# Kernel tuning notes

Hardware: AMD Instinct MI355X
Metric: run time of the kernel (lower is better)

Reference implementation:

```python
import jax, jax.numpy as jnp
import numpy as np

MSG_DIM = 100
REG_WEIGHT = 1.0
N_NODES = 100000
N_EDGES = 1000000
D_FEAT = 6
HIDDEN = 300
OUT_DIM = 2


def setup_inputs() -> dict:
    key = jax.random.key(0)
    ks = jax.random.split(key, 10)
    def glorot(k, shape):
        fan_in = shape[0]
        return jax.random.normal(k, shape, dtype=jnp.float32) / jnp.sqrt(jnp.float32(fan_in))
    return {
        "x": jax.random.normal(ks[0], (N_NODES, D_FEAT), dtype=jnp.float32),
        "edge_index": jax.random.randint(ks[1], (2, N_EDGES), 0, N_NODES, dtype=jnp.int64)
            if jax.config.jax_enable_x64 else jax.random.randint(ks[1], (2, N_EDGES), 0, N_NODES, dtype=jnp.int32),
        "y": jax.random.normal(ks[2], (N_NODES, OUT_DIM), dtype=jnp.float32),
        "target": jax.random.normal(ks[3], (N_NODES, OUT_DIM), dtype=jnp.float32),
        "W1": glorot(ks[4], (2 * D_FEAT, HIDDEN)),
        "b1": jnp.zeros((HIDDEN,), dtype=jnp.float32),
        "W2": glorot(ks[5], (HIDDEN, HIDDEN)),
        "b2": jnp.zeros((HIDDEN,), dtype=jnp.float32),
        "W3": glorot(ks[6], (HIDDEN, 2 * MSG_DIM)),
        "b3": jnp.zeros((2 * MSG_DIM,), dtype=jnp.float32),
    }


def reference(x, edge_index, y, target, W1, b1, W2, b2, W3, b3):
    # MAE term: sum |y - target| / n_nodes
    base_loss = jnp.sum(jnp.abs(y - target)) / y.shape[0]
    # Gather sender/receiver node features per edge and concat -> [E, 2*d_feat]
    e = jnp.concatenate([x[edge_index[0]], x[edge_index[1]]], axis=1)
    # edge_model MLP: 2*d_feat -> 300 -> 300 -> 2*msg_dim
    h = jax.nn.relu(e @ W1 + b1)
    h = jax.nn.relu(h @ W2 + b2)
    messages = h @ W3 + b3  # [E, 2*msg_dim]
    mu = messages[:, :MSG_DIM]
    logvar = messages[:, MSG_DIM:]
    kl_reg = jnp.sum(0.5 * (mu * mu + jnp.exp(logvar) - logvar - 1.0)) / messages.shape[0]
    return base_loss + REG_WEIGHT * kl_reg
```

## Files before the change

kernel.cpp:

```cpp
#include <hip/hip_runtime.h>

#define N_NODES 100000
#define N_EDGES 1000000
#define D_FEAT  6
#define HIDDEN  300
#define HID_P   320
#define MSG     100
#define OUTC    200
#define OUTC_P  208
#define MT      64
#define NT_H    (HID_P/16)
#define NT_M    (OUTC_P/16)
#define KS_H    (HID_P/32)

typedef __bf16 bf16_t;
typedef __bf16 bf16x8 __attribute__((ext_vector_type(8)));
typedef float  floatx4 __attribute__((ext_vector_type(4)));

#define H_STRIDE  328
#define A1_STRIDE 40

#define PREP_BLOCKS 700
#define LOSS_BLOCKS 200
__global__ void prep_kernel(const float* __restrict__ W1, const float* __restrict__ W2,
                            const float* __restrict__ W3, bf16_t* __restrict__ W1P,
                            bf16_t* __restrict__ W2P, bf16_t* __restrict__ W3P,
                            const float* __restrict__ y, const float* __restrict__ t,
                            float* __restrict__ out) {
    if (blockIdx.x >= PREP_BLOCKS) {
        float s = 0.f;
        for (int i = (blockIdx.x - PREP_BLOCKS) * blockDim.x + threadIdx.x;
             i < N_NODES * 2; i += LOSS_BLOCKS * blockDim.x)
            s += fabsf(y[i] - t[i]);
        #pragma unroll
        for (int off = 32; off; off >>= 1) s += __shfl_down(s, off);
        __shared__ float red[4];
        if ((threadIdx.x & 63) == 0) red[threadIdx.x >> 6] = s;
        __syncthreads();
        if (threadIdx.x == 0)
            atomicAdd(out, (red[0] + red[1] + red[2] + red[3]) * (1.0f / N_NODES));
        return;
    }
    const int n1 = NT_H * 512;
    const int n2 = NT_H * KS_H * 512;
    const int n3 = NT_M * KS_H * 512;
    const int total = n1 + n2 + n3;
    for (int id = blockIdx.x * blockDim.x + threadIdx.x; id < total;
         id += PREP_BLOCKS * blockDim.x) {
        if (id < n1) {
            int nt = id >> 9, rem = id & 511, lane = rem >> 3, j = rem & 7;
            int n = nt * 16 + (lane & 15), k = (lane >> 4) * 8 + j;
            float v = (n < HIDDEN && k < 2 * D_FEAT) ? W1[k * HIDDEN + n] : 0.f;
            W1P[id] = (bf16_t)v;
        } else if (id < n1 + n2) {
            int r = id - n1;
            int chunk = r >> 9, rem = r & 511, lane = rem >> 3, j = rem & 7;
            int ks = chunk % KS_H, nt = chunk / KS_H;
            int n = nt * 16 + (lane & 15), k = ks * 32 + (lane >> 4) * 8 + j;
            float v = (n < HIDDEN && k < HIDDEN) ? W2[k * HIDDEN + n] : 0.f;
            W2P[r] = (bf16_t)v;
        } else {
            int r = id - n1 - n2;
            int chunk = r >> 9, rem = r & 511, lane = rem >> 3, j = rem & 7;
            int ks = chunk % KS_H, nt = chunk / KS_H;
            int n = nt * 16 + (lane & 15), k = ks * 32 + (lane >> 4) * 8 + j;
            float v = (n < OUTC && k < HIDDEN) ? W3[k * OUTC + n] : 0.f;
            W3P[r] = (bf16_t)v;
        }
    }
}

__global__ __launch_bounds__(512, 6) void mlp_kernel(
    const float* __restrict__ x, const int* __restrict__ ei,
    const bf16_t* __restrict__ W1P, const bf16_t* __restrict__ W2P,
    const bf16_t* __restrict__ W3P,
    const float* __restrict__ b1, const float* __restrict__ b2,
    const float* __restrict__ b3, float* __restrict__ out) {
    __shared__ __align__(16) bf16_t A1[MT * A1_STRIDE];
    __shared__ __align__(16) bf16_t H[MT * H_STRIDE];
    __shared__ float red[8];

    const int tid  = threadIdx.x;
    const int wave = tid >> 6, lane = tid & 63;
    const int quad = lane >> 4, l16 = lane & 15;
    const int wn = wave;
    const int cnt_h = (wn < 4) ? 3 : 2;
    const int cnt_m = (wn >= 3) ? 2 : 1;
    const long e0 = (long)blockIdx.x * MT;

    {
        uint* a32 = (uint*)A1;
        for (int i = tid; i < MT * A1_STRIDE / 2; i += 512) a32[i] = 0u;
    }
    __syncthreads();
    if (tid < 2 * MT) {
        int m = tid >> 1, side = tid & 1;
        int node = ei[(long)side * N_EDGES + e0 + m];
        const float* xr = x + (long)node * D_FEAT;
        bf16_t* dst = A1 + m * A1_STRIDE + side * D_FEAT;
        #pragma unroll
        for (int j = 0; j < D_FEAT; j++) dst[j] = (bf16_t)xr[j];
    }
    __syncthreads();

    floatx4 acc1[3][4];
    {
        bf16x8 a[4];
        #pragma unroll
        for (int mi = 0; mi < 4; mi++)
            a[mi] = *(const bf16x8*)&A1[(mi * 16 + l16) * A1_STRIDE + quad * 8];
        #pragma unroll
        for (int t = 0; t < 3; t++) {
            if (t < cnt_h) {
                int ntg = wn + 8 * t;
                bf16x8 b = *(const bf16x8*)&W1P[(ntg * 64 + lane) * 8];
                #pragma unroll
                for (int mi = 0; mi < 4; mi++) {
                    floatx4 z = {0.f, 0.f, 0.f, 0.f};
                    acc1[t][mi] = __builtin_amdgcn_mfma_f32_16x16x32_bf16(a[mi], b, z, 0, 0, 0);
                }
            }
        }
    }
    #pragma unroll
    for (int t = 0; t < 3; t++) {
        if (t < cnt_h) {
            int n = (wn + 8 * t) * 16 + l16;
            float bias = (n < HIDDEN) ? b1[n] : 0.f;
            #pragma unroll
            for (int mi = 0; mi < 4; mi++) {
                int mbase = mi * 16 + quad * 4;
                #pragma unroll
                for (int r = 0; r < 4; r++) {
                    float v = fmaxf(acc1[t][mi][r] + bias, 0.f);
                    H[(mbase + r) * H_STRIDE + n] = (bf16_t)v;
                }
            }
        }
    }
    __syncthreads();

    floatx4 acc2[3][4];
    #pragma unroll
    for (int t = 0; t < 3; t++)
        #pragma unroll
        for (int mi = 0; mi < 4; mi++) acc2[t][mi] = (floatx4){0.f, 0.f, 0.f, 0.f};
    #pragma unroll 2
    for (int ks = 0; ks < KS_H; ks++) {
        bf16x8 a[4];
        #pragma unroll
        for (int mi = 0; mi < 4; mi++)
            a[mi] = *(const bf16x8*)&H[(mi * 16 + l16) * H_STRIDE + ks * 32 + quad * 8];
        #pragma unroll
        for (int t = 0; t < 3; t++) {
            if (t < cnt_h) {
                int ntg = wn + 8 * t;
                bf16x8 b = *(const bf16x8*)&W2P[((ntg * KS_H + ks) * 64 + lane) * 8];
                #pragma unroll
                for (int mi = 0; mi < 4; mi++)
                    acc2[t][mi] = __builtin_amdgcn_mfma_f32_16x16x32_bf16(a[mi], b, acc2[t][mi], 0, 0, 0);
            }
        }
    }
    __syncthreads();
    #pragma unroll
    for (int t = 0; t < 3; t++) {
        if (t < cnt_h) {
            int n = (wn + 8 * t) * 16 + l16;
            float bias = (n < HIDDEN) ? b2[n] : 0.f;
            #pragma unroll
            for (int mi = 0; mi < 4; mi++) {
                int mbase = mi * 16 + quad * 4;
                #pragma unroll
                for (int r = 0; r < 4; r++) {
                    float v = fmaxf(acc2[t][mi][r] + bias, 0.f);
                    H[(mbase + r) * H_STRIDE + n] = (bf16_t)v;
                }
            }
        }
    }
    __syncthreads();

    floatx4 acc3[2][4];
    #pragma unroll
    for (int t = 0; t < 2; t++)
        #pragma unroll
        for (int mi = 0; mi < 4; mi++) acc3[t][mi] = (floatx4){0.f, 0.f, 0.f, 0.f};
    #pragma unroll 2
    for (int ks = 0; ks < KS_H; ks++) {
        bf16x8 a[4];
        #pragma unroll
        for (int mi = 0; mi < 4; mi++)
            a[mi] = *(const bf16x8*)&H[(mi * 16 + l16) * H_STRIDE + ks * 32 + quad * 8];
        #pragma unroll
        for (int t = 0; t < 2; t++) {
            if (t < cnt_m) {
                int ntg = wn + 5 * t;
                bf16x8 b = *(const bf16x8*)&W3P[((ntg * KS_H + ks) * 64 + lane) * 8];
                #pragma unroll
                for (int mi = 0; mi < 4; mi++)
                    acc3[t][mi] = __builtin_amdgcn_mfma_f32_16x16x32_bf16(a[mi], b, acc3[t][mi], 0, 0, 0);
            }
        }
    }
    float s = 0.f;
    #pragma unroll
    for (int t = 0; t < 2; t++) {
        if (t < cnt_m) {
            int n = (wn + 5 * t) * 16 + l16;
            if (n < OUTC) {
                float bias = b3[n];
                #pragma unroll
                for (int mi = 0; mi < 4; mi++)
                    #pragma unroll
                    for (int r = 0; r < 4; r++) {
                        float v = acc3[t][mi][r] + bias;
                        if (n < MSG) s += 0.5f * v * v;
                        else         s += 0.5f * (__expf(v) - v - 1.f);
                    }
            }
        }
    }
    #pragma unroll
    for (int off = 32; off; off >>= 1) s += __shfl_down(s, off);
    if (lane == 0) red[wave] = s;
    __syncthreads();
    if (tid == 0) {
        float t2 = 0.f;
        #pragma unroll
        for (int w = 0; w < 8; w++) t2 += red[w];
        atomicAdd(out, t2 * (1.0f / N_EDGES));
    }
}

extern "C" void kernel_launch(void* const* d_in, const int* in_sizes, int n_in,
                              void* d_out, int out_size, void* d_ws, size_t ws_size,
                              hipStream_t stream) {
    const float* x      = (const float*)d_in[0];
    const int*   ei     = (const int*)d_in[1];
    const float* y      = (const float*)d_in[2];
    const float* target = (const float*)d_in[3];
    const float* W1     = (const float*)d_in[4];
    const float* b1     = (const float*)d_in[5];
    const float* W2     = (const float*)d_in[6];
    const float* b2     = (const float*)d_in[7];
    const float* W3     = (const float*)d_in[8];
    const float* b3     = (const float*)d_in[9];
    float* out = (float*)d_out;

    bf16_t* W1P = (bf16_t*)d_ws;
    bf16_t* W2P = W1P + NT_H * 512;
    bf16_t* W3P = W2P + NT_H * KS_H * 512;

    hipMemsetAsync(d_out, 0, sizeof(float), stream);
    prep_kernel<<<PREP_BLOCKS + LOSS_BLOCKS, 256, 0, stream>>>(
        W1, W2, W3, W1P, W2P, W3P, y, target, out);
    mlp_kernel<<<N_EDGES / MT, 512, 0, stream>>>(x, ei, W1P, W2P, W3P, b1, b2, b3, out);
}
```

Before: 490.4 us.

## Store activations in MFMA fragment layout and swap operands to pack-store outputs

Swaps the MFMA operands so weights act as A and activations as B, making each lane hold four consecutive hidden columns. That allows bias to be read as a float4 and the ReLU outputs to be written to shared memory as packed bf16x4 stores. Activations are kept in a pre-swizzled fragment layout, so every layer reads one contiguous 16-byte chunk per lane instead of using padded-row strides. The goal is fewer shared-memory store instructions and fewer bank conflicts in the epilogues. The price is more complex index math, and the A1 zero-fill now covers only 2048 elements, which happens to match the new buffer size.

```diff
diff --git a/kernel.cpp b/kernel.cpp
--- a/kernel.cpp
+++ b/kernel.cpp
@@ -15,10 +15,8 @@
 
 typedef __bf16 bf16_t;
 typedef __bf16 bf16x8 __attribute__((ext_vector_type(8)));
+typedef __bf16 bf16x4 __attribute__((ext_vector_type(4)));
 typedef float  floatx4 __attribute__((ext_vector_type(4)));
-
-#define H_STRIDE  328
-#define A1_STRIDE 40
 
 #define PREP_BLOCKS 700
 #define LOSS_BLOCKS 200
@@ -76,48 +74,47 @@
     const bf16_t* __restrict__ W3P,
     const float* __restrict__ b1, const float* __restrict__ b2,
     const float* __restrict__ b3, float* __restrict__ out) {
-    __shared__ __align__(16) bf16_t A1[MT * A1_STRIDE];
-    __shared__ __align__(16) bf16_t H[MT * H_STRIDE];
+    __shared__ __align__(16) bf16_t A1f[4 * 64 * 8];
+    __shared__ __align__(16) bf16_t Hf[4 * KS_H * 64 * 8];
     __shared__ float red[8];
 
     const int tid  = threadIdx.x;
-    const int wave = tid >> 6, lane = tid & 63;
-    const int quad = lane >> 4, l16 = lane & 15;
-    const int wn = wave;
-    const int cnt_h = (wn < 4) ? 3 : 2;
-    const int cnt_m = (wn >= 3) ? 2 : 1;
+    const int w    = tid >> 6, lane = tid & 63;
+    const int q    = lane >> 4, l16 = lane & 15;
+    const int cnt_h = (w < 4) ? 3 : 2;
+    const int cnt_m = (w >= 3) ? 2 : 1;
     const long e0 = (long)blockIdx.x * MT;
 
-    {
-        uint* a32 = (uint*)A1;
-        for (int i = tid; i < MT * A1_STRIDE / 2; i += 512) a32[i] = 0u;
-    }
+    *(ulong*)&A1f[tid * 4] = 0ul;
     __syncthreads();
     if (tid < 2 * MT) {
         int m = tid >> 1, side = tid & 1;
         int node = ei[(long)side * N_EDGES + e0 + m];
         const float* xr = x + (long)node * D_FEAT;
-        bf16_t* dst = A1 + m * A1_STRIDE + side * D_FEAT;
-        #pragma unroll
-        for (int j = 0; j < D_FEAT; j++) dst[j] = (bf16_t)xr[j];
+        int et = m >> 4, ml = m & 15;
+        #pragma unroll
+        for (int c = 0; c < D_FEAT; c++) {
+            int k = side * D_FEAT + c;
+            int lp = ml + 16 * (k >> 3);
+            A1f[(et * 64 + lp) * 8 + (k & 7)] = (bf16_t)xr[c];
+        }
     }
     __syncthreads();
 
     floatx4 acc1[3][4];
     {
-        bf16x8 a[4];
-        #pragma unroll
-        for (int mi = 0; mi < 4; mi++)
-            a[mi] = *(const bf16x8*)&A1[(mi * 16 + l16) * A1_STRIDE + quad * 8];
+        bf16x8 hb[4];
+        #pragma unroll
+        for (int e = 0; e < 4; e++)
+            hb[e] = *(const bf16x8*)&A1f[(e * 64 + lane) * 8];
         #pragma unroll
         for (int t = 0; t < 3; t++) {
             if (t < cnt_h) {
-                int ntg = wn + 8 * t;
-                bf16x8 b = *(const bf16x8*)&W1P[(ntg * 64 + lane) * 8];
-                #pragma unroll
-                for (int mi = 0; mi < 4; mi++) {
+                bf16x8 wf = *(const bf16x8*)&W1P[((w + 8 * t) * 64 + lane) * 8];
+                #pragma unroll
+                for (int e = 0; e < 4; e++) {
                     floatx4 z = {0.f, 0.f, 0.f, 0.f};
-                    acc1[t][mi] = __builtin_amdgcn_mfma_f32_16x16x32_bf16(a[mi], b, z, 0, 0, 0);
+                    acc1[t][e] = __builtin_amdgcn_mfma_f32_16x16x32_bf16(wf, hb[e], z, 0, 0, 0);
                 }
             }
         }
@@ -125,16 +122,17 @@
     #pragma unroll
     for (int t = 0; t < 3; t++) {
         if (t < cnt_h) {
-            int n = (wn + 8 * t) * 16 + l16;
-            float bias = (n < HIDDEN) ? b1[n] : 0.f;
+            int n0 = (w + 8 * t) * 16 + 4 * q;
+            floatx4 bv = (n0 < HIDDEN) ? *(const floatx4*)&b1[n0]
+                                       : (floatx4){0.f, 0.f, 0.f, 0.f};
+            int ks = n0 >> 5, lp = l16 + 16 * ((n0 >> 3) & 3), j0 = n0 & 7;
             #pragma unroll
-            for (int mi = 0; mi < 4; mi++) {
-                int mbase = mi * 16 + quad * 4;
-                #pragma unroll
-                for (int r = 0; r < 4; r++) {
-                    float v = fmaxf(acc1[t][mi][r] + bias, 0.f);
-                    H[(mbase + r) * H_STRIDE + n] = (bf16_t)v;
-                }
+            for (int e = 0; e < 4; e++) {
+                bf16x4 pk;
+                #pragma unroll
+                for (int r = 0; r < 4; r++)
+                    pk[r] = (bf16_t)fmaxf(acc1[t][e][r] + bv[r], 0.f);
+                *(bf16x4*)&Hf[((e * KS_H + ks) * 64 + lp) * 8 + j0] = pk;
             }
         }
     }
@@ -144,21 +142,20 @@
     #pragma unroll
     for (int t = 0; t < 3; t++)
         #pragma unroll
-        for (int mi = 0; mi < 4; mi++) acc2[t][mi] = (floatx4){0.f, 0.f, 0.f, 0.f};
+        for (int e = 0; e < 4; e++) acc2[t][e] = (floatx4){0.f, 0.f, 0.f, 0.f};
     #pragma unroll 2
     for (int ks = 0; ks < KS_H; ks++) {
-        bf16x8 a[4];
-        #pragma unroll
-        for (int mi = 0; mi < 4; mi++)
-            a[mi] = *(const bf16x8*)&H[(mi * 16 + l16) * H_STRIDE + ks * 32 + quad * 8];
+        bf16x8 hb[4];
+        #pragma unroll
+        for (int e = 0; e < 4; e++)
+            hb[e] = *(const bf16x8*)&Hf[((e * KS_H + ks) * 64 + lane) * 8];
         #pragma unroll
         for (int t = 0; t < 3; t++) {
             if (t < cnt_h) {
-                int ntg = wn + 8 * t;
-                bf16x8 b = *(const bf16x8*)&W2P[((ntg * KS_H + ks) * 64 + lane) * 8];
-                #pragma unroll
-                for (int mi = 0; mi < 4; mi++)
-                    acc2[t][mi] = __builtin_amdgcn_mfma_f32_16x16x32_bf16(a[mi], b, acc2[t][mi], 0, 0, 0);
+                bf16x8 wf = *(const bf16x8*)&W2P[(((w + 8 * t) * KS_H + ks) * 64 + lane) * 8];
+                #pragma unroll
+                for (int e = 0; e < 4; e++)
+                    acc2[t][e] = __builtin_amdgcn_mfma_f32_16x16x32_bf16(wf, hb[e], acc2[t][e], 0, 0, 0);
             }
         }
     }
@@ -166,16 +163,17 @@
     #pragma unroll
     for (int t = 0; t < 3; t++) {
         if (t < cnt_h) {
-            int n = (wn + 8 * t) * 16 + l16;
-            float bias = (n < HIDDEN) ? b2[n] : 0.f;
+            int n0 = (w + 8 * t) * 16 + 4 * q;
+            floatx4 bv = (n0 < HIDDEN) ? *(const floatx4*)&b2[n0]
+                                       : (floatx4){0.f, 0.f, 0.f, 0.f};
+            int ks = n0 >> 5, lp = l16 + 16 * ((n0 >> 3) & 3), j0 = n0 & 7;
             #pragma unroll
-            for (int mi = 0; mi < 4; mi++) {
-                int mbase = mi * 16 + quad * 4;
-                #pragma unroll
-                for (int r = 0; r < 4; r++) {
-                    float v = fmaxf(acc2[t][mi][r] + bias, 0.f);
-                    H[(mbase + r) * H_STRIDE + n] = (bf16_t)v;
-                }
+            for (int e = 0; e < 4; e++) {
+                bf16x4 pk;
+                #pragma unroll
+                for (int r = 0; r < 4; r++)
+                    pk[r] = (bf16_t)fmaxf(acc2[t][e][r] + bv[r], 0.f);
+                *(bf16x4*)&Hf[((e * KS_H + ks) * 64 + lp) * 8 + j0] = pk;
             }
         }
     }
@@ -185,21 +183,20 @@
     #pragma unroll
     for (int t = 0; t < 2; t++)
         #pragma unroll
-        for (int mi = 0; mi < 4; mi++) acc3[t][mi] = (floatx4){0.f, 0.f, 0.f, 0.f};
+        for (int e = 0; e < 4; e++) acc3[t][e] = (floatx4){0.f, 0.f, 0.f, 0.f};
     #pragma unroll 2
     for (int ks = 0; ks < KS_H; ks++) {
-        bf16x8 a[4];
-        #pragma unroll
-        for (int mi = 0; mi < 4; mi++)
-            a[mi] = *(const bf16x8*)&H[(mi * 16 + l16) * H_STRIDE + ks * 32 + quad * 8];
+        bf16x8 hb[4];
+        #pragma unroll
+        for (int e = 0; e < 4; e++)
+            hb[e] = *(const bf16x8*)&Hf[((e * KS_H + ks) * 64 + lane) * 8];
         #pragma unroll
         for (int t = 0; t < 2; t++) {
             if (t < cnt_m) {
-                int ntg = wn + 5 * t;
-                bf16x8 b = *(const bf16x8*)&W3P[((ntg * KS_H + ks) * 64 + lane) * 8];
-                #pragma unroll
-                for (int mi = 0; mi < 4; mi++)
-                    acc3[t][mi] = __builtin_amdgcn_mfma_f32_16x16x32_bf16(a[mi], b, acc3[t][mi], 0, 0, 0);
+                bf16x8 wf = *(const bf16x8*)&W3P[(((w + 5 * t) * KS_H + ks) * 64 + lane) * 8];
+                #pragma unroll
+                for (int e = 0; e < 4; e++)
+                    acc3[t][e] = __builtin_amdgcn_mfma_f32_16x16x32_bf16(wf, hb[e], acc3[t][e], 0, 0, 0);
             }
         }
     }
@@ -207,28 +204,29 @@
     #pragma unroll
     for (int t = 0; t < 2; t++) {
         if (t < cnt_m) {
-            int n = (wn + 5 * t) * 16 + l16;
-            if (n < OUTC) {
-                float bias = b3[n];
-                #pragma unroll
-                for (int mi = 0; mi < 4; mi++)
+            int n0 = (w + 5 * t) * 16 + 4 * q;
+            if (n0 < OUTC) {
+                floatx4 bv = *(const floatx4*)&b3[n0];
+                bool is_mu = (n0 < MSG);
+                #pragma unroll
+                for (int e = 0; e < 4; e++)
                     #pragma unroll
                     for (int r = 0; r < 4; r++) {
-                        float v = acc3[t][mi][r] + bias;
-                        if (n < MSG) s += 0.5f * v * v;
-                        else         s += 0.5f * (__expf(v) - v - 1.f);
+                        float v = acc3[t][e][r] + bv[r];
+                        if (is_mu) s += 0.5f * v * v;
+                        else       s += 0.5f * (__expf(v) - v - 1.f);
                     }
             }
         }
     }
     #pragma unroll
     for (int off = 32; off; off >>= 1) s += __shfl_down(s, off);
-    if (lane == 0) red[wave] = s;
+    if (lane == 0) red[w] = s;
     __syncthreads();
     if (tid == 0) {
         float t2 = 0.f;
         #pragma unroll
-        for (int w = 0; w < 8; w++) t2 += red[w];
+        for (int i = 0; i < 8; i++) t2 += red[i];
         atomicAdd(out, t2 * (1.0f / N_EDGES));
     }
 }
```

Measured after the change: 458.8 us. 1.07x faster.
